# Kernel tuning notes

Measured on AMD Instinct MI355X. Metric: run time of the kernel, lower is better.

Reference implementation:

```python
import jax, jax.numpy as jnp
import numpy as np

N_U, N_M, E, H, L = 200000, 50000, 600000, 128, 2


def segment_mean(x, idx, n):
    s = jax.ops.segment_sum(x, idx, num_segments=n)
    d = jax.ops.segment_sum(jnp.ones((x.shape[0], 1), x.dtype), idx, num_segments=n)
    return s / jnp.maximum(d, 1.0)


def setup_inputs() -> dict:
    key = jax.random.key(0)
    ks = iter(jax.random.split(key, 40))
    g = lambda shape, scale: jax.random.normal(next(ks), shape, jnp.float32) * scale
    inp = {
        "user_x": g((N_U, 3), 1.0),
        "merchant_x": g((N_M, 2), 1.0),
        "edge_attr": g((E, 2), 1.0),
        "user_lin_w": g((3, H), 3 ** -0.5), "user_lin_b": jnp.zeros((H,), jnp.float32),
        "merchant_lin_w": g((2, H), 2 ** -0.5), "merchant_lin_b": jnp.zeros((H,), jnp.float32),
        "edge_lin_w": g((2, H), 2 ** -0.5), "edge_lin_b": jnp.zeros((H,), jnp.float32),
        # SAGEConv per layer, per relation: out = lin_l(mean_j x_j) + lin_r(x_dst)
        "conv_u2m_wl": g((L, H, H), H ** -0.5), "conv_u2m_bl": jnp.zeros((L, H), jnp.float32),
        "conv_u2m_wr": g((L, H, H), H ** -0.5),
        "conv_m2u_wl": g((L, H, H), H ** -0.5), "conv_m2u_bl": jnp.zeros((L, H), jnp.float32),
        "conv_m2u_wr": g((L, H, H), H ** -0.5),
        "c1_w": g((3 * H, H), (3 * H) ** -0.5), "c1_b": jnp.zeros((H,), jnp.float32),
        "c2_w": g((H, 1), H ** -0.5), "c2_b": jnp.zeros((1,), jnp.float32),
        "edge_index": jnp.stack([
            jax.random.randint(next(ks), (E,), 0, N_U),
            jax.random.randint(next(ks), (E,), 0, N_M),
        ]).astype(jnp.int64),
    }
    return inp


def reference(user_x, merchant_x, edge_attr,
              user_lin_w, user_lin_b, merchant_lin_w, merchant_lin_b,
              edge_lin_w, edge_lin_b,
              conv_u2m_wl, conv_u2m_bl, conv_u2m_wr,
              conv_m2u_wl, conv_m2u_bl, conv_m2u_wr,
              c1_w, c1_b, c2_w, c2_b, edge_index):
    relu = jax.nn.relu
    src, dst = edge_index[0], edge_index[1]  # user -> merchant

    h_u = relu(user_x @ user_lin_w + user_lin_b)        # [N_U, H]
    h_m = relu(merchant_x @ merchant_lin_w + merchant_lin_b)  # [N_M, H]
    e = relu(edge_attr @ edge_lin_w + edge_lin_b)       # [E, H]

    for l in range(L):
        # user -> merchant SAGEConv
        agg_m = segment_mean(h_u[src], dst, N_M)
        new_m = agg_m @ conv_u2m_wl[l] + conv_u2m_bl[l] + h_m @ conv_u2m_wr[l]
        # merchant -> user SAGEConv (reverse edges)
        agg_u = segment_mean(h_m[dst], src, N_U)
        new_u = agg_u @ conv_m2u_wl[l] + conv_m2u_bl[l] + h_u @ conv_m2u_wr[l]
        h_u, h_m = relu(new_u), relu(new_m)

    # vectorized form of the per-edge gather-concat-MLP loop
    feats = jnp.concatenate([h_u[src], h_m[dst], e], axis=-1)  # [E, 3H]
    hid = relu(feats @ c1_w + c1_b)  # dropout skipped (eval mode)
    out = hid @ c2_w + c2_b          # [E, 1]
    return out.squeeze(-1)           # [E]
```

## Files before the change

kernel.cpp:

```cpp
#include <hip/hip_runtime.h>

#define H   128
#define NU  200000
#define NM  50000
#define NE  600000

typedef __attribute__((ext_vector_type(8))) short bf16x8;
typedef __attribute__((ext_vector_type(4))) float f32x4;
typedef unsigned short ushort_t;
typedef unsigned int uint_t;

__device__ __forceinline__ ushort_t f2bf(float x) {
    uint_t b = __float_as_uint(x);
    return (ushort_t)((b + 0x7FFF + ((b >> 16) & 1)) >> 16);
}

__device__ __forceinline__ void gload16(const void* gsrc, void* lds_base) {
    __builtin_amdgcn_global_load_lds(
        (const __attribute__((address_space(1))) unsigned int*)gsrc,
        (__attribute__((address_space(3))) unsigned int*)lds_base,
        16, 0, 0);
}

__global__ void __launch_bounds__(256)
encode_bf16_kernel(const float* __restrict__ x, const float* __restrict__ W,
                   const float* __restrict__ b, ushort_t* __restrict__ h,
                   int n, int K) {
    int idx = blockIdx.x * 256 + threadIdx.x;
    if (idx >= n * 16) return;
    int r = idx >> 4, c0 = (idx & 15) * 8;
    float4 ba = *(const float4*)&b[c0], bb = *(const float4*)&b[c0 + 4];
    float acc[8] = {ba.x, ba.y, ba.z, ba.w, bb.x, bb.y, bb.z, bb.w};
    for (int k = 0; k < K; k++) {
        float xv = x[r * K + k];
        float4 wa = *(const float4*)&W[k * H + c0], wb = *(const float4*)&W[k * H + c0 + 4];
        acc[0] = fmaf(xv, wa.x, acc[0]); acc[1] = fmaf(xv, wa.y, acc[1]);
        acc[2] = fmaf(xv, wa.z, acc[2]); acc[3] = fmaf(xv, wa.w, acc[3]);
        acc[4] = fmaf(xv, wb.x, acc[4]); acc[5] = fmaf(xv, wb.y, acc[5]);
        acc[6] = fmaf(xv, wb.z, acc[6]); acc[7] = fmaf(xv, wb.w, acc[7]);
    }
    union { ushort_t u[8]; uint4 q; } pk;
#pragma unroll
    for (int j = 0; j < 8; j++) pk.u[j] = f2bf(fmaxf(acc[j], 0.f));
    *(uint4*)&h[(size_t)r * H + c0] = pk.q;
}

__global__ void count_kernel(const int* __restrict__ ei, int* cu, int* cm, int n) {
    int e = blockIdx.x * blockDim.x + threadIdx.x;
    if (e >= n) return;
    atomicAdd(&cu[ei[e]], 1);
    atomicAdd(&cm[ei[NE + e]], 1);
}

__global__ void __launch_bounds__(256)
scanA_kernel(const int* __restrict__ cnt, int* __restrict__ bsum, int n) {
    __shared__ int s[256];
    int b = blockIdx.x, t = threadIdx.x;
    int base = b * 2048 + t * 8;
    int sum = 0;
    if (base + 8 <= n) {
        int4 a = *(const int4*)&cnt[base];
        int4 c = *(const int4*)&cnt[base + 4];
        sum = a.x + a.y + a.z + a.w + c.x + c.y + c.z + c.w;
    } else {
        for (int j = 0; j < 8; j++) { int i = base + j; if (i < n) sum += cnt[i]; }
    }
    s[t] = sum;
    __syncthreads();
    for (int off = 128; off >= 1; off >>= 1) {
        if (t < off) s[t] += s[t + off];
        __syncthreads();
    }
    if (t == 0) bsum[b] = s[0];
}

__global__ void __launch_bounds__(256)
scanB_kernel(const int* __restrict__ bsum, int* __restrict__ boff, int nb,
             int* __restrict__ rp_total) {
    __shared__ int s[256];
    int t = threadIdx.x;
    int v = (t < nb) ? bsum[t] : 0;
    s[t] = v;
    __syncthreads();
    for (int off = 1; off < 256; off <<= 1) {
        int x = (t >= off) ? s[t - off] : 0;
        __syncthreads();
        s[t] += x;
        __syncthreads();
    }
    if (t < nb) boff[t] = s[t] - v;
    if (t == 255) rp_total[0] = s[255];
}

__global__ void __launch_bounds__(256)
scanC_kernel(const int* __restrict__ cnt, const int* __restrict__ boff,
             int* __restrict__ rp, int n) {
    __shared__ int s[256];
    int b = blockIdx.x, t = threadIdx.x;
    int base = b * 2048 + t * 8;
    int v[8];
    int sum = 0;
    if (base + 8 <= n) {
        int4 a = *(const int4*)&cnt[base];
        int4 c = *(const int4*)&cnt[base + 4];
        v[0] = a.x; v[1] = a.y; v[2] = a.z; v[3] = a.w;
        v[4] = c.x; v[5] = c.y; v[6] = c.z; v[7] = c.w;
#pragma unroll
        for (int j = 0; j < 8; j++) sum += v[j];
    } else {
#pragma unroll
        for (int j = 0; j < 8; j++) { int i = base + j; v[j] = (i < n) ? cnt[i] : 0; sum += v[j]; }
    }
    s[t] = sum;
    __syncthreads();
    for (int off = 1; off < 256; off <<= 1) {
        int x = (t >= off) ? s[t - off] : 0;
        __syncthreads();
        s[t] += x;
        __syncthreads();
    }
    int run = boff[b] + s[t] - sum;
    if (base + 8 <= n) {
        int o[8];
#pragma unroll
        for (int j = 0; j < 8; j++) { o[j] = run; run += v[j]; }
        *(int4*)&rp[base]     = make_int4(o[0], o[1], o[2], o[3]);
        *(int4*)&rp[base + 4] = make_int4(o[4], o[5], o[6], o[7]);
    } else {
#pragma unroll
        for (int j = 0; j < 8; j++) { int i = base + j; if (i < n) rp[i] = run; run += v[j]; }
    }
}

__global__ void fill_kernel(const int* __restrict__ ei, const int* __restrict__ rpu,
                            const int* __restrict__ rpm, int* cu, int* cm,
                            int* __restrict__ eu, int* __restrict__ em,
                            int* __restrict__ us, int* __restrict__ ue, int n) {
    int e = blockIdx.x * blockDim.x + threadIdx.x;
    if (e >= n) return;
    int s = ei[e], d = ei[NE + e];
    int slot = rpu[s] + atomicAdd(&cu[s], 1);
    eu[slot] = d;
    us[slot] = s;
    ue[slot] = e;
    em[rpm[d] + atomicAdd(&cm[d], 1)] = s;
}

__global__ void __launch_bounds__(256)
agg_both_kernel(const ushort_t* __restrict__ pu, const ushort_t* __restrict__ pm,
                const int* __restrict__ rpu, const int* __restrict__ rpm,
                const int* __restrict__ eu, const int* __restrict__ em,
                ushort_t* __restrict__ qu, ushort_t* __restrict__ qm, int nbM) {
    int bid = blockIdx.x;
    const ushort_t* src; const int* rp; const int* nbl; ushort_t* dst; int node, n;
    if (bid < nbM) {
        node = bid * 4 + (threadIdx.x >> 6); n = NM; src = pu; rp = rpm; nbl = em; dst = qm;
    } else {
        node = (bid - nbM) * 4 + (threadIdx.x >> 6); n = NU; src = pm; rp = rpu; nbl = eu; dst = qu;
    }
    if (node >= n) return;
    int lane = threadIdx.x & 63;
    int beg = rp[node], end = rp[node + 1];
    float a0 = 0.f, a1 = 0.f;
    int j = beg;
    for (; j + 4 <= end; j += 4) {
        int n0 = nbl[j], n1 = nbl[j + 1], n2 = nbl[j + 2], n3 = nbl[j + 3];
        uint_t v0 = *(const uint_t*)&src[(size_t)n0 * H + lane * 2];
        uint_t v1 = *(const uint_t*)&src[(size_t)n1 * H + lane * 2];
        uint_t v2 = *(const uint_t*)&src[(size_t)n2 * H + lane * 2];
        uint_t v3 = *(const uint_t*)&src[(size_t)n3 * H + lane * 2];
        a0 += (__uint_as_float((v0 & 0xffffu) << 16) + __uint_as_float((v1 & 0xffffu) << 16))
            + (__uint_as_float((v2 & 0xffffu) << 16) + __uint_as_float((v3 & 0xffffu) << 16));
        a1 += (__uint_as_float(v0 & 0xffff0000u) + __uint_as_float(v1 & 0xffff0000u))
            + (__uint_as_float(v2 & 0xffff0000u) + __uint_as_float(v3 & 0xffff0000u));
    }
    for (; j < end; j++) {
        uint_t v = *(const uint_t*)&src[(size_t)nbl[j] * H + lane * 2];
        a0 += __uint_as_float((v & 0xffffu) << 16);
        a1 += __uint_as_float(v & 0xffff0000u);
    }
    int deg = end - beg;
    float inv = 1.0f / (float)(deg > 1 ? deg : 1);
    uint_t r = (uint_t)f2bf(a0 * inv) | ((uint_t)f2bf(a1 * inv) << 16);
    *(uint_t*)&dst[(size_t)node * H + lane * 2] = r;
}

__global__ void convert_w_kernel(const float* __restrict__ c1w, ushort_t* __restrict__ outT) {
    int i = blockIdx.x * 256 + threadIdx.x;
    if (i >= 384 * 128) return;
    int k = i >> 7, n = i & 127;
    outT[n * 384 + k] = f2bf(c1w[i]);
}

__global__ void convert_conv_w_kernel(const float* __restrict__ wl, const float* __restrict__ wr,
                                      ushort_t* __restrict__ outT) {
    int i = blockIdx.x * 256 + threadIdx.x;
    if (i >= 128 * 256) return;
    int col = i >> 8, k = i & 255;
    float v = (k < 128) ? wl[k * H + col] : wr[(k - 128) * H + col];
    outT[i] = f2bf(v);
}

__global__ void __launch_bounds__(512)
conv_pair_kernel(const ushort_t* __restrict__ aggM, const ushort_t* __restrict__ selfM,
                 const ushort_t* __restrict__ wTm, const float* __restrict__ blm,
                 ushort_t* __restrict__ outM,
                 const ushort_t* __restrict__ aggU, const ushort_t* __restrict__ selfU,
                 const ushort_t* __restrict__ wTu, const float* __restrict__ blu,
                 ushort_t* __restrict__ outU, int ntM) {
    const ushort_t *agg, *self, *wT; const float* bl; ushort_t* out; int n, tile;
    if ((int)blockIdx.x < ntM) {
        tile = blockIdx.x; agg = aggM; self = selfM; wT = wTm; bl = blm; out = outM; n = NM;
    } else {
        tile = blockIdx.x - ntM; agg = aggU; self = selfU; wT = wTu; bl = blu; out = outU; n = NU;
    }
    int node0 = tile * 64;
    int t = threadIdx.x, lane = t & 63, w = t >> 6;
    int l15 = lane & 15, koff = lane >> 4;
    __shared__ ushort_t As[64 * 256];
    char* Ab = (char*)As;

#pragma unroll
    for (int it = 0; it < 4; it++) {
        int row = it * 16 + w * 2 + (lane >> 5);
        int node = node0 + row; if (node >= n) node = n - 1;
        int g = (lane & 31) ^ (row & 7);
        const ushort_t* src = (g < 16) ? &agg[(size_t)node * H + g * 8]
                                       : &self[(size_t)node * H + (g - 16) * 8];
        gload16(src, Ab + it * 8192 + w * 1024);
    }

    bf16x8 bw[8];
    int col = w * 16 + l15;
#pragma unroll
    for (int ks = 0; ks < 8; ks++)
        bw[ks] = *reinterpret_cast<const bf16x8*>(&wT[col * 256 + ks * 32 + koff * 8]);
    float bias0 = bl[col];
    int sw = l15 & 7;
    __syncthreads();

    f32x4 acc[4];
#pragma unroll
    for (int rg = 0; rg < 4; rg++) acc[rg] = (f32x4){bias0, bias0, bias0, bias0};
#pragma unroll
    for (int ks = 0; ks < 8; ks++) {
#pragma unroll
        for (int rg = 0; rg < 4; rg++) {
            int row = rg * 16 + l15;
            const bf16x8 a = *reinterpret_cast<const bf16x8*>(
                Ab + row * 512 + (((ks * 4 + koff) ^ sw) << 4));
            acc[rg] = __builtin_amdgcn_mfma_f32_16x16x32_bf16(a, bw[ks], acc[rg], 0, 0, 0);
        }
    }

#pragma unroll
    for (int rg = 0; rg < 4; rg++)
#pragma unroll
        for (int reg = 0; reg < 4; reg++) {
            int node = node0 + rg * 16 + koff * 4 + reg;
            if (node < n)
                out[(size_t)node * H + col] = f2bf(fmaxf(acc[rg][reg], 0.f));
        }
}

__global__ void __launch_bounds__(512)
edge_mlp_mfma_kernel(const ushort_t* __restrict__ h_u, const ushort_t* __restrict__ h_m,
                     const float* __restrict__ ea, const float* __restrict__ ew,
                     const float* __restrict__ ebias,
                     const ushort_t* __restrict__ c1wT, const float* __restrict__ c1b,
                     const float* __restrict__ c2w, const float* __restrict__ c2b,
                     const int* __restrict__ us, const int* __restrict__ eu,
                     const int* __restrict__ ue, float* __restrict__ out) {
    const int ET = 64;
    int nwg = gridDim.x;
    int q = nwg >> 3, r = nwg & 7;
    int xcd = blockIdx.x & 7, pos = blockIdx.x >> 3;
    int tile = (xcd < r ? xcd * (q + 1) : r * (q + 1) + (xcd - r) * q) + pos;
    int e0 = tile * ET;

    int t = threadIdx.x;
    int lane = t & 63, w = t >> 6;
    int l15 = lane & 15, koff = lane >> 4;

    __shared__ ushort_t As1[ET * 256];
    __shared__ ushort_t As2[ET * 128];
    __shared__ float part[8 * ET];
    __shared__ int se[ET], de[ET], ee[ET];
    char* Ab1 = (char*)As1;
    char* Ab2 = (char*)As2;

    if (t < ET) {
        se[t] = us[e0 + t];
        de[t] = eu[e0 + t];
        ee[t] = ue[e0 + t];
    }
    __syncthreads();

#pragma unroll
    for (int it = 0; it < 4; it++) {
        int row = it * 16 + w * 2 + (lane >> 5);
        int g = (lane & 31) ^ (row & 7);
        const ushort_t* src = (g < 16) ? &h_u[(size_t)se[row] * H + g * 8]
                                       : &h_m[(size_t)de[row] * H + (g - 16) * 8];
        gload16(src, Ab1 + it * 8192 + w * 1024);
    }

    bf16x8 bf_[12];
    int col = w * 16 + l15;
#pragma unroll
    for (int ks = 0; ks < 12; ks++)
        bf_[ks] = *reinterpret_cast<const bf16x8*>(&c1wT[col * 384 + ks * 32 + koff * 8]);

#pragma unroll
    for (int it = 0; it < 2; it++) {
        int lin = it * 512 + t;
        int row = lin >> 4, g2 = lin & 15;
        int c = g2 * 8;
        int eid = ee[row];
        float a0 = ea[(size_t)eid * 2], a1 = ea[(size_t)eid * 2 + 1];
        float4 w0a = *(const float4*)&ew[c];
        float4 w0b = *(const float4*)&ew[c + 4];
        float4 w1a = *(const float4*)&ew[H + c];
        float4 w1b = *(const float4*)&ew[H + c + 4];
        float4 bba = *(const float4*)&ebias[c];
        float4 bbb = *(const float4*)&ebias[c + 4];
        float v[8];
        v[0] = fmaxf(fmaf(a0, w0a.x, fmaf(a1, w1a.x, bba.x)), 0.f);
        v[1] = fmaxf(fmaf(a0, w0a.y, fmaf(a1, w1a.y, bba.y)), 0.f);
        v[2] = fmaxf(fmaf(a0, w0a.z, fmaf(a1, w1a.z, bba.z)), 0.f);
        v[3] = fmaxf(fmaf(a0, w0a.w, fmaf(a1, w1a.w, bba.w)), 0.f);
        v[4] = fmaxf(fmaf(a0, w0b.x, fmaf(a1, w1b.x, bbb.x)), 0.f);
        v[5] = fmaxf(fmaf(a0, w0b.y, fmaf(a1, w1b.y, bbb.y)), 0.f);
        v[6] = fmaxf(fmaf(a0, w0b.z, fmaf(a1, w1b.z, bbb.z)), 0.f);
        v[7] = fmaxf(fmaf(a0, w0b.w, fmaf(a1, w1b.w, bbb.w)), 0.f);
        union { ushort_t u[8]; uint4 q; } pk;
#pragma unroll
        for (int j = 0; j < 8; j++) pk.u[j] = f2bf(v[j]);
        *(uint4*)(Ab2 + row * 256 + ((g2 ^ (row & 7)) << 4)) = pk.q;
    }
    __syncthreads();

    int sw = l15 & 7;
    float bias0 = c1b[col];
    f32x4 acc[4];
#pragma unroll
    for (int rg = 0; rg < 4; rg++) acc[rg] = (f32x4){bias0, bias0, bias0, bias0};
#pragma unroll
    for (int ks = 0; ks < 12; ks++) {
#pragma unroll
        for (int rg = 0; rg < 4; rg++) {
            int row = rg * 16 + l15;
            const bf16x8 a = (ks < 8)
                ? *reinterpret_cast<const bf16x8*>(Ab1 + row * 512 + (((ks * 4 + koff) ^ sw) << 4))
                : *reinterpret_cast<const bf16x8*>(Ab2 + row * 256 + ((((ks - 8) * 4 + koff) ^ sw) << 4));
            acc[rg] = __builtin_amdgcn_mfma_f32_16x16x32_bf16(a, bf_[ks], acc[rg], 0, 0, 0);
        }
    }

    float c2v = c2w[col];
#pragma unroll
    for (int rg = 0; rg < 4; rg++) {
#pragma unroll
        for (int reg = 0; reg < 4; reg++) {
            float p = fmaxf(acc[rg][reg], 0.f) * c2v;
#pragma unroll
            for (int off = 8; off >= 1; off >>= 1) p += __shfl_xor(p, off, 64);
            if (l15 == 0) part[w * ET + rg * 16 + koff * 4 + reg] = p;
        }
    }
    __syncthreads();
    if (t < ET) {
        float s = part[t];
#pragma unroll
        for (int ww = 1; ww < 8; ww++) s += part[ww * ET + t];
        out[ee[t]] = s + c2b[0];
    }
}

extern "C" void kernel_launch(void* const* d_in, const int* in_sizes, int n_in,
                              void* d_out, int out_size, void* d_ws, size_t ws_size,
                              hipStream_t stream) {
    const float* user_x     = (const float*)d_in[0];
    const float* merchant_x = (const float*)d_in[1];
    const float* edge_attr  = (const float*)d_in[2];
    const float* user_w     = (const float*)d_in[3];
    const float* user_b     = (const float*)d_in[4];
    const float* merch_w    = (const float*)d_in[5];
    const float* merch_b    = (const float*)d_in[6];
    const float* edge_w     = (const float*)d_in[7];
    const float* edge_b     = (const float*)d_in[8];
    const float* u2m_wl     = (const float*)d_in[9];
    const float* u2m_bl     = (const float*)d_in[10];
    const float* u2m_wr     = (const float*)d_in[11];
    const float* m2u_wl     = (const float*)d_in[12];
    const float* m2u_bl     = (const float*)d_in[13];
    const float* m2u_wr     = (const float*)d_in[14];
    const float* c1w        = (const float*)d_in[15];
    const float* c1b        = (const float*)d_in[16];
    const float* c2w        = (const float*)d_in[17];
    const float* c2b        = (const float*)d_in[18];
    const int*   ei         = (const int*)d_in[19];
    float* out = (float*)d_out;

    ushort_t* hu   = (ushort_t*)d_ws;
    ushort_t* hm   = hu  + (size_t)NU * H;
    ushort_t* hu2  = hm  + (size_t)NM * H;
    ushort_t* hm2  = hu2 + (size_t)NU * H;
    ushort_t* c1wT = hm2 + (size_t)NM * H;
    ushort_t* wTc  = c1wT + 384 * 128;
    int* rpu = (int*)(wTc + 4 * 128 * 256);
    int* rpm = rpu + (NU + 1);
    int* cu  = rpm + (NM + 1);
    int* cm  = cu + NU;
    int* eu  = cm + NM;
    int* em  = eu + NE;
    int* us  = em + NE;
    int* ue  = us + NE;
    int* bsum_u = ue + NE;
    int* boff_u = bsum_u + 128;
    int* bsum_m = boff_u + 128;
    int* boff_m = bsum_m + 128;

    const int NBU = (NU + 2047) / 2048;
    const int NBM = (NM + 2047) / 2048;

    hipMemsetAsync(cu, 0, (size_t)(NU + NM) * sizeof(int), stream);

    encode_bf16_kernel<<<(NU * 16 + 255) / 256, 256, 0, stream>>>(user_x, user_w, user_b, hu, NU, 3);
    encode_bf16_kernel<<<(NM * 16 + 255) / 256, 256, 0, stream>>>(merchant_x, merch_w, merch_b, hm, NM, 2);
    convert_w_kernel<<<(384 * 128 + 255) / 256, 256, 0, stream>>>(c1w, c1wT);
    for (int l = 0; l < 2; l++) {
        convert_conv_w_kernel<<<128, 256, 0, stream>>>(
            u2m_wl + (size_t)l * H * H, u2m_wr + (size_t)l * H * H, wTc + (size_t)l * 128 * 256);
        convert_conv_w_kernel<<<128, 256, 0, stream>>>(
            m2u_wl + (size_t)l * H * H, m2u_wr + (size_t)l * H * H, wTc + (size_t)(2 + l) * 128 * 256);
    }

    count_kernel<<<(NE + 255) / 256, 256, 0, stream>>>(ei, cu, cm, NE);
    scanA_kernel<<<NBU, 256, 0, stream>>>(cu, bsum_u, NU);
    scanB_kernel<<<1, 256, 0, stream>>>(bsum_u, boff_u, NBU, rpu + NU);
    scanC_kernel<<<NBU, 256, 0, stream>>>(cu, boff_u, rpu, NU);
    scanA_kernel<<<NBM, 256, 0, stream>>>(cm, bsum_m, NM);
    scanB_kernel<<<1, 256, 0, stream>>>(bsum_m, boff_m, NBM, rpm + NM);
    scanC_kernel<<<NBM, 256, 0, stream>>>(cm, boff_m, rpm, NM);
    hipMemsetAsync(cu, 0, (size_t)(NU + NM) * sizeof(int), stream);
    fill_kernel<<<(NE + 255) / 256, 256, 0, stream>>>(ei, rpu, rpm, cu, cm, eu, em, us, ue, NE);

    const int AGG_NBM = (NM + 3) / 4;
    const int AGG_NBU = (NU + 3) / 4;
    const int CONV_TILES_M = (NM + 63) / 64;
    const int CONV_TILES_U = (NU + 63) / 64;

    const ushort_t* pu = hu; const ushort_t* pm = hm;
    ushort_t* qu = hu2; ushort_t* qm = hm2;
    for (int l = 0; l < 2; l++) {
        agg_both_kernel<<<AGG_NBM + AGG_NBU, 256, 0, stream>>>(
            pu, pm, rpu, rpm, eu, em, qu, qm, AGG_NBM);
        conv_pair_kernel<<<CONV_TILES_M + CONV_TILES_U, 512, 0, stream>>>(
            qm, pm, wTc + (size_t)l * 128 * 256, u2m_bl + (size_t)l * H, qm,
            qu, pu, wTc + (size_t)(2 + l) * 128 * 256, m2u_bl + (size_t)l * H, qu,
            CONV_TILES_M);
        const ushort_t* tu = pu; pu = qu; qu = (ushort_t*)tu;
        const ushort_t* tm = pm; pm = qm; qm = (ushort_t*)tm;
    }

    edge_mlp_mfma_kernel<<<NE / 64, 512, 0, stream>>>(pu, pm, edge_attr, edge_w, edge_b,
                                                      c1wT, c1b, c2w, c2b, us, eu, ue, out);
}
```

Measured before the change: 629.2 us.

## Fuse neighbor mean aggregation into SAGE conv GEMM kernel via LDS

Removes the separate aggregation kernel and computes each node's neighbor mean inside the conv kernel, writing the bf16 result straight into a swizzled LDS tile that feeds the MFMA GEMM. This avoids writing the aggregated features to global memory and reading them back, and saves one launch per layer. In exchange, each conv block now runs gather latency serially before its GEMM (8 nodes per wave) with less parallelism per node than the standalone kernel.

Result: faster. 580.1 us (-7.8%).

```diff
diff --git a/kernel.cpp b/kernel.cpp
--- a/kernel.cpp
+++ b/kernel.cpp
@@ -146,45 +146,6 @@
     em[rpm[d] + atomicAdd(&cm[d], 1)] = s;
 }
 
-__global__ void __launch_bounds__(256)
-agg_both_kernel(const ushort_t* __restrict__ pu, const ushort_t* __restrict__ pm,
-                const int* __restrict__ rpu, const int* __restrict__ rpm,
-                const int* __restrict__ eu, const int* __restrict__ em,
-                ushort_t* __restrict__ qu, ushort_t* __restrict__ qm, int nbM) {
-    int bid = blockIdx.x;
-    const ushort_t* src; const int* rp; const int* nbl; ushort_t* dst; int node, n;
-    if (bid < nbM) {
-        node = bid * 4 + (threadIdx.x >> 6); n = NM; src = pu; rp = rpm; nbl = em; dst = qm;
-    } else {
-        node = (bid - nbM) * 4 + (threadIdx.x >> 6); n = NU; src = pm; rp = rpu; nbl = eu; dst = qu;
-    }
-    if (node >= n) return;
-    int lane = threadIdx.x & 63;
-    int beg = rp[node], end = rp[node + 1];
-    float a0 = 0.f, a1 = 0.f;
-    int j = beg;
-    for (; j + 4 <= end; j += 4) {
-        int n0 = nbl[j], n1 = nbl[j + 1], n2 = nbl[j + 2], n3 = nbl[j + 3];
-        uint_t v0 = *(const uint_t*)&src[(size_t)n0 * H + lane * 2];
-        uint_t v1 = *(const uint_t*)&src[(size_t)n1 * H + lane * 2];
-        uint_t v2 = *(const uint_t*)&src[(size_t)n2 * H + lane * 2];
-        uint_t v3 = *(const uint_t*)&src[(size_t)n3 * H + lane * 2];
-        a0 += (__uint_as_float((v0 & 0xffffu) << 16) + __uint_as_float((v1 & 0xffffu) << 16))
-            + (__uint_as_float((v2 & 0xffffu) << 16) + __uint_as_float((v3 & 0xffffu) << 16));
-        a1 += (__uint_as_float(v0 & 0xffff0000u) + __uint_as_float(v1 & 0xffff0000u))
-            + (__uint_as_float(v2 & 0xffff0000u) + __uint_as_float(v3 & 0xffff0000u));
-    }
-    for (; j < end; j++) {
-        uint_t v = *(const uint_t*)&src[(size_t)nbl[j] * H + lane * 2];
-        a0 += __uint_as_float((v & 0xffffu) << 16);
-        a1 += __uint_as_float(v & 0xffff0000u);
-    }
-    int deg = end - beg;
-    float inv = 1.0f / (float)(deg > 1 ? deg : 1);
-    uint_t r = (uint_t)f2bf(a0 * inv) | ((uint_t)f2bf(a1 * inv) << 16);
-    *(uint_t*)&dst[(size_t)node * H + lane * 2] = r;
-}
-
 __global__ void convert_w_kernel(const float* __restrict__ c1w, ushort_t* __restrict__ outT) {
     int i = blockIdx.x * 256 + threadIdx.x;
     if (i >= 384 * 128) return;
@@ -202,32 +163,65 @@
 }
 
 __global__ void __launch_bounds__(512)
-conv_pair_kernel(const ushort_t* __restrict__ aggM, const ushort_t* __restrict__ selfM,
+conv_pair_kernel(const ushort_t* __restrict__ hu_in, const ushort_t* __restrict__ hm_in,
+                 const int* __restrict__ rpu, const int* __restrict__ rpm,
+                 const int* __restrict__ eu, const int* __restrict__ em,
                  const ushort_t* __restrict__ wTm, const float* __restrict__ blm,
                  ushort_t* __restrict__ outM,
-                 const ushort_t* __restrict__ aggU, const ushort_t* __restrict__ selfU,
                  const ushort_t* __restrict__ wTu, const float* __restrict__ blu,
                  ushort_t* __restrict__ outU, int ntM) {
-    const ushort_t *agg, *self, *wT; const float* bl; ushort_t* out; int n, tile;
+    const ushort_t *nbr, *self, *wT; const float* bl; ushort_t* out;
+    const int *rp, *nbl; int n, tile;
     if ((int)blockIdx.x < ntM) {
-        tile = blockIdx.x; agg = aggM; self = selfM; wT = wTm; bl = blm; out = outM; n = NM;
+        tile = blockIdx.x; nbr = hu_in; self = hm_in; rp = rpm; nbl = em;
+        wT = wTm; bl = blm; out = outM; n = NM;
     } else {
-        tile = blockIdx.x - ntM; agg = aggU; self = selfU; wT = wTu; bl = blu; out = outU; n = NU;
+        tile = blockIdx.x - ntM; nbr = hm_in; self = hu_in; rp = rpu; nbl = eu;
+        wT = wTu; bl = blu; out = outU; n = NU;
     }
     int node0 = tile * 64;
     int t = threadIdx.x, lane = t & 63, w = t >> 6;
     int l15 = lane & 15, koff = lane >> 4;
-    __shared__ ushort_t As[64 * 256];
-    char* Ab = (char*)As;
-
-#pragma unroll
-    for (int it = 0; it < 4; it++) {
-        int row = it * 16 + w * 2 + (lane >> 5);
+    __shared__ ushort_t AsAgg[64 * 128];
+    __shared__ ushort_t AsSelf[64 * 128];
+    char* Aa = (char*)AsAgg;
+    char* Asf = (char*)AsSelf;
+
+#pragma unroll
+    for (int it = 0; it < 2; it++) {
+        int row = it * 32 + w * 4 + (lane >> 4);
         int node = node0 + row; if (node >= n) node = n - 1;
-        int g = (lane & 31) ^ (row & 7);
-        const ushort_t* src = (g < 16) ? &agg[(size_t)node * H + g * 8]
-                                       : &self[(size_t)node * H + (g - 16) * 8];
-        gload16(src, Ab + it * 8192 + w * 1024);
+        int g = (lane & 15) ^ (row & 7);
+        gload16(&self[(size_t)node * H + g * 8], Asf + it * 8192 + w * 1024);
+    }
+
+    for (int i = 0; i < 8; i++) {
+        int row = w * 8 + i;
+        int node = node0 + row;
+        float a0 = 0.f, a1 = 0.f;
+        int beg = 0, end = 0;
+        if (node < n) { beg = rp[node]; end = rp[node + 1]; }
+        int j = beg;
+        for (; j + 4 <= end; j += 4) {
+            int n0 = nbl[j], n1 = nbl[j + 1], n2 = nbl[j + 2], n3 = nbl[j + 3];
+            uint_t v0 = *(const uint_t*)&nbr[(size_t)n0 * H + lane * 2];
+            uint_t v1 = *(const uint_t*)&nbr[(size_t)n1 * H + lane * 2];
+            uint_t v2 = *(const uint_t*)&nbr[(size_t)n2 * H + lane * 2];
+            uint_t v3 = *(const uint_t*)&nbr[(size_t)n3 * H + lane * 2];
+            a0 += (__uint_as_float((v0 & 0xffffu) << 16) + __uint_as_float((v1 & 0xffffu) << 16))
+                + (__uint_as_float((v2 & 0xffffu) << 16) + __uint_as_float((v3 & 0xffffu) << 16));
+            a1 += (__uint_as_float(v0 & 0xffff0000u) + __uint_as_float(v1 & 0xffff0000u))
+                + (__uint_as_float(v2 & 0xffff0000u) + __uint_as_float(v3 & 0xffff0000u));
+        }
+        for (; j < end; j++) {
+            uint_t v = *(const uint_t*)&nbr[(size_t)nbl[j] * H + lane * 2];
+            a0 += __uint_as_float((v & 0xffffu) << 16);
+            a1 += __uint_as_float(v & 0xffff0000u);
+        }
+        int deg = end - beg;
+        float inv = 1.0f / (float)(deg > 1 ? deg : 1);
+        uint_t r = (uint_t)f2bf(a0 * inv) | ((uint_t)f2bf(a1 * inv) << 16);
+        *(uint_t*)(Aa + row * 256 + ((((lane >> 2)) ^ (row & 7)) << 4) + (lane & 3) * 4) = r;
     }
 
     bf16x8 bw[8];
@@ -247,8 +241,9 @@
 #pragma unroll
         for (int rg = 0; rg < 4; rg++) {
             int row = rg * 16 + l15;
-            const bf16x8 a = *reinterpret_cast<const bf16x8*>(
-                Ab + row * 512 + (((ks * 4 + koff) ^ sw) << 4));
+            const bf16x8 a = (ks < 4)
+                ? *reinterpret_cast<const bf16x8*>(Aa  + row * 256 + (((ks * 4 + koff) ^ sw) << 4))
+                : *reinterpret_cast<const bf16x8*>(Asf + row * 256 + ((((ks - 4) * 4 + koff) ^ sw) << 4));
             acc[rg] = __builtin_amdgcn_mfma_f32_16x16x32_bf16(a, bw[ks], acc[rg], 0, 0, 0);
         }
     }
@@ -446,19 +441,16 @@
     hipMemsetAsync(cu, 0, (size_t)(NU + NM) * sizeof(int), stream);
     fill_kernel<<<(NE + 255) / 256, 256, 0, stream>>>(ei, rpu, rpm, cu, cm, eu, em, us, ue, NE);
 
-    const int AGG_NBM = (NM + 3) / 4;
-    const int AGG_NBU = (NU + 3) / 4;
     const int CONV_TILES_M = (NM + 63) / 64;
     const int CONV_TILES_U = (NU + 63) / 64;
 
     const ushort_t* pu = hu; const ushort_t* pm = hm;
     ushort_t* qu = hu2; ushort_t* qm = hm2;
     for (int l = 0; l < 2; l++) {
-        agg_both_kernel<<<AGG_NBM + AGG_NBU, 256, 0, stream>>>(
-            pu, pm, rpu, rpm, eu, em, qu, qm, AGG_NBM);
         conv_pair_kernel<<<CONV_TILES_M + CONV_TILES_U, 512, 0, stream>>>(
-            qm, pm, wTc + (size_t)l * 128 * 256, u2m_bl + (size_t)l * H, qm,
-            qu, pu, wTc + (size_t)(2 + l) * 128 * 256, m2u_bl + (size_t)l * H, qu,
+            pu, pm, rpu, rpm, eu, em,
+            wTc + (size_t)l * 128 * 256, u2m_bl + (size_t)l * H, qm,
+            wTc + (size_t)(2 + l) * 128 * 256, m2u_bl + (size_t)l * H, qu,
             CONV_TILES_M);
         const ushort_t* tu = pu; pu = qu; qu = (ushort_t*)tu;
         const ushort_t* tm = pm; pm = qm; qm = (ushort_t*)tm;
```
